# Kernel tuning notes

Hardware: AMD Instinct MI355X
Metric: run time of the kernel (lower is better)

## Reference

```python
import jax, jax.numpy as jnp
import numpy as np

B, S, IN_DIM, CTX = 32, 512, 256, 128
D, H, L = 128, 4, 2
DH = D // H
HID = 512
TOTAL = 11 * D * D + 8 * D  # hypernet flat weight size per sample
EPS = 1e-5


def _layernorm(x, g, b):
    mu = jnp.mean(x, axis=-1, keepdims=True)
    var = jnp.mean(jnp.square(x - mu), axis=-1, keepdims=True)
    return (x - mu) * jax.lax.rsqrt(var + EPS) * g + b


def setup_inputs() -> dict:
    key = jax.random.key(0)
    ks = jax.random.split(key, 24)
    f32 = jnp.float32
    inp = {
        'x': jax.random.normal(ks[0], (B, S, IN_DIM), f32),
        'context_vector': jax.random.normal(ks[1], (B, CTX), f32),
        'in_proj_w': jax.random.normal(ks[2], (D, IN_DIM), f32) * (IN_DIM ** -0.5),
        'in_proj_b': jnp.zeros((D,), f32),
        'pe': jax.random.normal(ks[3], (1, S, D), f32) * 0.02,
        'hfc1_w': jax.random.normal(ks[4], (L, HID, CTX), f32) * (CTX ** -0.5),
        'hfc1_b': jnp.zeros((L, HID), f32),
        'hfc2_w': jax.random.normal(ks[5], (L, TOTAL, HID), f32) * 0.02,
        'hfc2_b': jnp.zeros((L, TOTAL), f32),
        'out_proj_w': jax.random.normal(ks[6], (L, D, D), f32) * (D ** -0.5),
        'out_proj_b': jnp.zeros((L, D), f32),
        'ln1_g': jnp.ones((L, D), f32), 'ln1_b': jnp.zeros((L, D), f32),
        'ln2_g': jnp.ones((L, D), f32), 'ln2_b': jnp.zeros((L, D), f32),
        'alpha1': jnp.full((L,), 0.5, f32), 'alpha2': jnp.full((L,), 0.5, f32),
        'head_w': jax.random.normal(ks[7], (1, D), f32) * (D ** -0.5),
        'head_b': jnp.zeros((1,), f32),
    }
    return inp


def reference(x, context_vector, in_proj_w, in_proj_b, pe, hfc1_w, hfc1_b,
              hfc2_w, hfc2_b, out_proj_w, out_proj_b, ln1_g, ln1_b,
              ln2_g, ln2_b, alpha1, alpha2, head_w, head_b):
    # input projection + learned positional encoding
    h = jnp.einsum('bsi,di->bsd', x, in_proj_w) + in_proj_b
    h = h + pe[:, :h.shape[1], :]

    # flat split offsets for hypernet output
    sizes = [3 * D * D, 3 * D, 4 * D * D, 4 * D, 4 * D * D, D]
    offs = np.concatenate([[0], np.cumsum(sizes)])

    for l in range(L):
        # hypernet: per-sample weights from context
        hid = jax.nn.relu(context_vector @ hfc1_w[l].T + hfc1_b[l])
        flat = hid @ hfc2_w[l].T + hfc2_b[l]  # [B, TOTAL]
        aw = flat[:, offs[0]:offs[1]].reshape(B, 3 * D, D)
        ab = flat[:, offs[1]:offs[2]]                     # [B, 3D]
        f1w = flat[:, offs[2]:offs[3]].reshape(B, 4 * D, D)
        f1b = flat[:, offs[3]:offs[4]]                    # [B, 4D]
        f2w = flat[:, offs[4]:offs[5]].reshape(B, D, 4 * D)
        f2b = flat[:, offs[5]:offs[6]]                    # [B, D]

        # per-sample QKV projection (grouped GEMM over batch)
        qkv = jnp.einsum('bsd,bed->bse', h, aw) + ab[:, None, :]
        q, k, v = jnp.split(qkv, 3, axis=-1)
        q = q.reshape(B, S, H, DH)
        k = k.reshape(B, S, H, DH)
        v = v.reshape(B, S, H, DH)
        scores = jnp.einsum('bqhd,bkhd->bhqk', q, k) / jnp.sqrt(jnp.float32(DH))
        attn = jax.nn.softmax(scores, axis=-1)
        ctx = jnp.einsum('bhqk,bkhd->bqhd', attn, v).reshape(B, S, D)
        attn_out = jnp.einsum('bsd,ed->bse', ctx, out_proj_w[l]) + out_proj_b[l]

        h = _layernorm(h + alpha1[l] * attn_out, ln1_g[l], ln1_b[l])

        # per-sample FFN
        ff = jax.nn.relu(jnp.einsum('bsd,bfd->bsf', h, f1w) + f1b[:, None, :])
        ff = jnp.einsum('bsf,bdf->bsd', ff, f2w) + f2b[:, None, :]

        h = _layernorm(h + alpha2[l] * ff, ln2_g[l], ln2_b[l])

    out = h[:, -1, :] @ head_w.T + head_b  # [B, 1]
    return out
```

## Files before the change

### kernel.cpp

```cpp
#include <hip/hip_runtime.h>
#include <hip/hip_bf16.h>

constexpr int B_    = 32;
constexpr int S_    = 512;
constexpr int INDIM = 256;
constexpr int KCTX  = 128;
constexpr int D_    = 128;
constexpr int H_    = 4;
constexpr int L_    = 2;
constexpr int HID_  = 512;
constexpr int TOTAL_ = 11 * D_ * D_ + 8 * D_;
constexpr int OFF_AB  = 3 * D_ * D_;
constexpr int OFF_F1W = OFF_AB + 3 * D_;
constexpr int OFF_F1B = OFF_F1W + 4 * D_ * D_;
constexpr int OFF_F2W = OFF_F1B + 4 * D_;
constexpr int OFF_F2B = OFF_F2W + 4 * D_ * D_;
constexpr int TP = 132;

typedef __attribute__((ext_vector_type(8))) short short8;
typedef __attribute__((ext_vector_type(4))) short short4v;
typedef __attribute__((ext_vector_type(2))) short short2v;
typedef __attribute__((ext_vector_type(4))) float f32x4;

#define MFMA16 __builtin_amdgcn_mfma_f32_16x16x32_bf16

__device__ __forceinline__ short f2bf(float f) {
  __hip_bfloat16 h = __float2bfloat16(f);
  return __builtin_bit_cast(short, h);
}
__device__ __forceinline__ float bf2f(short s) {
  __hip_bfloat16 h = __builtin_bit_cast(__hip_bfloat16, s);
  return __bfloat162float(h);
}
struct bfpair { short hi, lo; };
__device__ __forceinline__ bfpair split2p(float x) {
  bfpair p;
  p.hi = f2bf(x);
  p.lo = f2bf(x - bf2f(p.hi));
  return p;
}

__device__ __forceinline__ void cvt_body(const float* __restrict__ in,
                                         short* __restrict__ oh,
                                         short* __restrict__ ol,
                                         int ktShift, int n8, int t) {
  if (t >= n8) return;
  int kt = 1 << ktShift;
  int row = t >> ktShift;
  int kc = t & (kt - 1);
  const float* p = in + ((long)row << (ktShift + 3)) + kc * 8;
  float4 v0 = *(const float4*)p;
  float4 v1 = *(const float4*)(p + 4);
  short8 h8, l8; bfpair q;
  q = split2p(v0.x); h8[0] = q.hi; l8[0] = q.lo;
  q = split2p(v0.y); h8[1] = q.hi; l8[1] = q.lo;
  q = split2p(v0.z); h8[2] = q.hi; l8[2] = q.lo;
  q = split2p(v0.w); h8[3] = q.hi; l8[3] = q.lo;
  q = split2p(v1.x); h8[4] = q.hi; l8[4] = q.lo;
  q = split2p(v1.y); h8[5] = q.hi; l8[5] = q.lo;
  q = split2p(v1.z); h8[6] = q.hi; l8[6] = q.lo;
  q = split2p(v1.w); h8[7] = q.hi; l8[7] = q.lo;
  long o = ((long)(row >> 4) * kt + kc) * 128 + (row & 15) * 8;
  *(short8*)(oh + o) = h8;
  *(short8*)(ol + o) = l8;
}

__global__ __launch_bounds__(256) void k_prep(
    const float* __restrict__ x, const float* __restrict__ ipw,
    const float* __restrict__ opw,
    short* __restrict__ xFh, short* __restrict__ xFl,
    short* __restrict__ ipwFh, short* __restrict__ ipwFl,
    short* __restrict__ opwFh, short* __restrict__ opwFl,
    const float* __restrict__ cvec, const float* __restrict__ h1w,
    const float* __restrict__ h1b,
    short* __restrict__ hidFh, short* __restrict__ hidFl) {
  int id = blockIdx.x, tid = threadIdx.x;
  if (id < 2048) {
    cvt_body(x, xFh, xFl, 5, B_ * S_ * INDIM / 8, id * 256 + tid);
  } else if (id < 2064) {
    cvt_body(ipw, ipwFh, ipwFl, 5, D_ * INDIM / 8, (id - 2048) * 256 + tid);
  } else if (id < 2080) {
    cvt_body(opw, opwFh, opwFl, 4, L_ * D_ * D_ / 8, (id - 2064) * 256 + tid);
  } else {
    int hb = id - 2080;
    int l = hb >> 5, b = hb & 31;
    __shared__ float cs[KCTX];
    if (tid < KCTX) cs[tid] = cvec[b * KCTX + tid];
    __syncthreads();
    #pragma unroll
    for (int jj = 0; jj < 2; ++jj) {
      int j = tid + jj * 256;
      const float* wr = h1w + (long)(l * HID_ + j) * KCTX;
      float s = h1b[l * HID_ + j];
      #pragma unroll
      for (int c = 0; c < KCTX; c += 4) {
        float4 cv = *(const float4*)(cs + c);
        float4 wv = *(const float4*)(wr + c);
        s += cv.x * wv.x + cv.y * wv.y + cv.z * wv.z + cv.w * wv.w;
      }
      s = fmaxf(s, 0.f);
      bfpair p = split2p(s);
      long o = (long)l * 32 * HID_ + ((long)(b >> 4) * 64 + (j >> 3)) * 128
             + (b & 15) * 8 + (j & 7);
      hidFh[o] = p.hi;
      hidFl[o] = p.lo;
    }
  }
}

__device__ void inproj_block(int id,
    const short* __restrict__ xFh, const short* __restrict__ xFl,
    const short* __restrict__ ipwFh, const short* __restrict__ ipwFl,
    const float* __restrict__ ipb, const float* __restrict__ pe,
    float* __restrict__ h_f, short* __restrict__ hFh, short* __restrict__ hFl) {
  const int tid = threadIdx.x, wave = tid >> 6, lane = tid & 63;
  const int r = lane & 15, g = lane >> 4;
  const int bx = id >> 5, b = id & 31;
  const int m0 = bx * 64 + (wave & 1) * 32;
  const int n0 = (wave >> 1) * 64;
  const long KT = (long)INDIM * 16;
  const short* pAh = xFh + (long)b * S_ * INDIM + (m0 >> 4) * KT + g * 128 + r * 8;
  const short* pAl = xFl + (long)b * S_ * INDIM + (m0 >> 4) * KT + g * 128 + r * 8;
  const short* pWh = ipwFh + (n0 >> 4) * KT + g * 128 + r * 8;
  const short* pWl = ipwFl + (n0 >> 4) * KT + g * 128 + r * 8;
  f32x4 acc[2][4] = {{{0,0,0,0},{0,0,0,0},{0,0,0,0},{0,0,0,0}},
                     {{0,0,0,0},{0,0,0,0},{0,0,0,0},{0,0,0,0}}};
  for (int kk = 0; kk < INDIM / 32; ++kk) {
    long ko = (long)kk * 512;
    short8 a0h = *(const short8*)(pAh + ko);
    short8 a1h = *(const short8*)(pAh + KT + ko);
    short8 a0l = *(const short8*)(pAl + ko);
    short8 a1l = *(const short8*)(pAl + KT + ko);
    #pragma unroll
    for (int ns = 0; ns < 4; ++ns) {
      short8 wh = *(const short8*)(pWh + ns * KT + ko);
      short8 wl = *(const short8*)(pWl + ns * KT + ko);
      acc[0][ns] = MFMA16(a0h, wl, acc[0][ns], 0, 0, 0);
      acc[0][ns] = MFMA16(a0l, wh, acc[0][ns], 0, 0, 0);
      acc[0][ns] = MFMA16(a0h, wh, acc[0][ns], 0, 0, 0);
      acc[1][ns] = MFMA16(a1h, wl, acc[1][ns], 0, 0, 0);
      acc[1][ns] = MFMA16(a1l, wh, acc[1][ns], 0, 0, 0);
      acc[1][ns] = MFMA16(a1h, wh, acc[1][ns], 0, 0, 0);
    }
  }
  #pragma unroll
  for (int ms = 0; ms < 2; ++ms) {
    #pragma unroll
    for (int ns = 0; ns < 4; ++ns) {
      int ccol = n0 + ns * 16 + r;
      float bv = ipb[ccol];
      #pragma unroll
      for (int reg = 0; reg < 4; ++reg) {
        int crow = m0 + ms * 16 + g * 4 + reg;
        float v = acc[ms][ns][reg] + bv + pe[crow * D_ + ccol];
        h_f[((long)b * S_ + crow) * D_ + ccol] = v;
        long o = (long)b * 65536 + (long)(crow >> 4) * 2048
               + (ccol >> 3) * 128 + (crow & 15) * 8 + (ccol & 7);
        bfpair sp = split2p(v);
        hFh[o] = sp.hi;
        hFl[o] = sp.lo;
      }
    }
  }
}

__global__ __launch_bounds__(256) void k_flat_ip(
    const short* __restrict__ hidh, const short* __restrict__ hidl,
    const float* __restrict__ W, const float* __restrict__ bias,
    short* __restrict__ awh, short* __restrict__ awl,
    short* __restrict__ f1h, short* __restrict__ f1l,
    short* __restrict__ f2h, short* __restrict__ f2l,
    float* __restrict__ ab, float* __restrict__ f1b, float* __restrict__ f2b,
    const short* __restrict__ xFh, const short* __restrict__ xFl,
    const short* __restrict__ ipwFh, const short* __restrict__ ipwFl,
    const float* __restrict__ ipb, const float* __restrict__ pe,
    float* __restrict__ h_f, short* __restrict__ hFh, short* __restrict__ hFl) {
  __shared__ short wls[2][64 * 64];
  const int id = blockIdx.x;
  if (id < 256) {
    inproj_block(id, xFh, xFl, ipwFh, ipwFl, ipb, pe, h_f, hFh, hFl);
    return;
  }
  const int fid = id - 256;
  const int l = fid / 2832;
  const int bxf = fid % 2832;
  hidh += (long)l * 32 * HID_;
  hidl += (long)l * 32 * HID_;
  W    += (long)l * TOTAL_ * HID_;
  bias += (long)l * TOTAL_;
  awh  += (long)l * B_ * 49152;  awl += (long)l * B_ * 49152;
  f1h  += (long)l * B_ * 65536;  f1l += (long)l * B_ * 65536;
  f2h  += (long)l * B_ * 65536;  f2l += (long)l * B_ * 65536;
  ab   += l * B_ * 384;  f1b += l * B_ * 512;  f2b += l * B_ * 128;
  const int tid = threadIdx.x, wave = tid >> 6, lane = tid & 63;
  const int r = lane & 15, g = lane >> 4;
  const int nb0 = bxf * 64;
  const int rr = tid >> 4;
  const int cc = (tid & 15) * 4;
  const float* wbase = W + (long)nb0 * HID_;
  float4 wv[2][4];
  #pragma unroll
  for (int rnd = 0; rnd < 4; ++rnd) {
    wv[0][rnd] = *(const float4*)(wbase + (long)(rnd * 16 + rr) * HID_ + cc);
    wv[1][rnd] = *(const float4*)(wbase + (long)(rnd * 16 + rr) * HID_ + 64 + cc);
  }
  const short* pAh = hidh + g * 128 + r * 8;
  const short* pAl = hidl + g * 128 + r * 8;
  f32x4 acc0 = {0, 0, 0, 0}, acc1 = {0, 0, 0, 0};
  int cur = 0;
  for (int c0 = 0; c0 < 512; c0 += 64) {
    #pragma unroll
    for (int rnd = 0; rnd < 4; ++rnd) {
      int row = rnd * 16 + rr;
      short4v h4, l4; bfpair q;
      q = split2p(wv[cur][rnd].x); h4[0] = q.hi; l4[0] = q.lo;
      q = split2p(wv[cur][rnd].y); h4[1] = q.hi; l4[1] = q.lo;
      q = split2p(wv[cur][rnd].z); h4[2] = q.hi; l4[2] = q.lo;
      q = split2p(wv[cur][rnd].w); h4[3] = q.hi; l4[3] = q.lo;
      int sb = row * 128 + ((cc * 2) ^ ((row & 7) << 4));
      *(short4v*)((char*)&wls[0][0] + sb) = h4;
      *(short4v*)((char*)&wls[1][0] + sb) = l4;
    }
    if (c0 + 128 < 512) {
      #pragma unroll
      for (int rnd = 0; rnd < 4; ++rnd)
        wv[cur][rnd] = *(const float4*)(wbase + (long)(rnd * 16 + rr) * HID_ + (c0 + 128) + cc);
    }
    __syncthreads();
    #pragma unroll
    for (int kk = 0; kk < 2; ++kk) {
      long ao = (long)(c0 * 16) + kk * 512;
      short8 ah0 = *(const short8*)(pAh + ao);
      short8 ah1 = *(const short8*)(pAh + 8192 + ao);
      short8 al0 = *(const short8*)(pAl + ao);
      short8 al1 = *(const short8*)(pAl + 8192 + ao);
      int wrow = wave * 16 + r;
      int wb = wrow * 128 + ((kk * 64 + g * 16) ^ ((r & 7) << 4));
      short8 wh = *(const short8*)((char*)&wls[0][0] + wb);
      short8 wl = *(const short8*)((char*)&wls[1][0] + wb);
      acc0 = MFMA16(ah0, wl, acc0, 0, 0, 0);
      acc0 = MFMA16(al0, wh, acc0, 0, 0, 0);
      acc0 = MFMA16(ah0, wh, acc0, 0, 0, 0);
      acc1 = MFMA16(ah1, wl, acc1, 0, 0, 0);
      acc1 = MFMA16(al1, wh, acc1, 0, 0, 0);
      acc1 = MFMA16(ah1, wh, acc1, 0, 0, 0);
    }
    __syncthreads();
    cur ^= 1;
  }
  constexpr int TPF = 68;
  float* tile = (float*)&wls[0][0];
  {
    float bv = bias[nb0 + wave * 16 + r];
    int col = wave * 16 + r;
    #pragma unroll
    for (int reg = 0; reg < 4; ++reg) {
      tile[(g * 4 + reg) * TPF + col]      = acc0[reg] + bv;
      tile[(g * 4 + reg + 16) * TPF + col] = acc1[reg] + bv;
    }
  }
  __syncthreads();
  {
    int b  = tid >> 3;
    int cg = tid & 7;
    int t0 = nb0 + cg * 8;
    float v[8];
    #pragma unroll
    for (int j = 0; j < 8; ++j) v[j] = tile[b * TPF + cg * 8 + j];
    if (t0 < OFF_AB) {
      int e = t0 >> 7, d = t0 & 127;
      long a = (long)b * 49152 + ((long)(e >> 4) * 16 + (d >> 3)) * 128 + (e & 15) * 8;
      short8 h8, l8; bfpair q;
      #pragma unroll
      for (int j = 0; j < 8; ++j) { q = split2p(v[j]); h8[j] = q.hi; l8[j] = q.lo; }
      *(short8*)(awh + a) = h8;
      *(short8*)(awl + a) = l8;
    } else if (t0 < OFF_F1W) {
      float* dst = ab + b * 384 + (t0 - OFF_AB);
      float4 x0 = {v[0], v[1], v[2], v[3]}, x1 = {v[4], v[5], v[6], v[7]};
      *(float4*)dst = x0; *(float4*)(dst + 4) = x1;
    } else if (t0 < OFF_F1B) {
      int i = t0 - OFF_F1W; int f = i >> 7, d = i & 127;
      long a = (long)b * 65536 + ((long)(f >> 4) * 16 + (d >> 3)) * 128 + (f & 15) * 8;
      short8 h8, l8; bfpair q;
      #pragma unroll
      for (int j = 0; j < 8; ++j) { q = split2p(v[j]); h8[j] = q.hi; l8[j] = q.lo; }
      *(short8*)(f1h + a) = h8;
      *(short8*)(f1l + a) = l8;
    } else if (t0 < OFF_F2W) {
      float* dst = f1b + b * 512 + (t0 - OFF_F1B);
      float4 x0 = {v[0], v[1], v[2], v[3]}, x1 = {v[4], v[5], v[6], v[7]};
      *(float4*)dst = x0; *(float4*)(dst + 4) = x1;
    } else if (t0 < OFF_F2B) {
      int i = t0 - OFF_F2W; int dd = i >> 9, f = i & 511;
      long a = (long)b * 65536 + ((long)(dd >> 4) * 64 + (f >> 3)) * 128 + (dd & 15) * 8;
      short8 h8, l8; bfpair q;
      #pragma unroll
      for (int j = 0; j < 8; ++j) { q = split2p(v[j]); h8[j] = q.hi; l8[j] = q.lo; }
      *(short8*)(f2h + a) = h8;
      *(short8*)(f2l + a) = l8;
    } else {
      float* dst = f2b + b * 128 + (t0 - OFF_F2B);
      float4 x0 = {v[0], v[1], v[2], v[3]}, x1 = {v[4], v[5], v[6], v[7]};
      *(float4*)dst = x0; *(float4*)(dst + 4) = x1;
    }
  }
}

template <int K, int EPI, bool RELU>
__global__ __launch_bounds__(256) void k_gemm(
    const short* __restrict__ Ah, const short* __restrict__ Al, long sA,
    const short* __restrict__ Wh, const short* __restrict__ Wl, long sW,
    const float* __restrict__ biasP, long sB,
    void* __restrict__ p0, void* __restrict__ p1,
    void* __restrict__ p2, void* __restrict__ p3,
    int N,
    const float* __restrict__ lng, const float* __restrict__ lnb,
    const float* __restrict__ lnal, int mOff, int nOff, int mode) {
  extern __shared__ char smem_dyn[];
  const int tid = threadIdx.x, wave = tid >> 6, lane = tid & 63;
  const int r = lane & 15, g = lane >> 4;
  const int b = blockIdx.z;
  int bx, by;
  if (mode == 1) {
    int xx = blockIdx.x;
    if (xx < 16) { bx = xx >> 1; by = 1 + (xx & 1); }
    else         { bx = 7; by = 0; }
  } else {
    bx = blockIdx.x + mOff; by = blockIdx.y + nOff;
  }
  const int m0 = bx * 64 + (wave & 1) * 32;
  const int n0 = by * 128 + (wave >> 1) * 64;
  const long KT = (long)K * 16;
  const short* pAh = Ah + (long)b * sA + (m0 >> 4) * KT + g * 128 + r * 8;
  const short* pAl = Al + (long)b * sA + (m0 >> 4) * KT + g * 128 + r * 8;
  const short* pWh = Wh + (long)b * sW + (n0 >> 4) * KT + g * 128 + r * 8;
  const short* pWl = Wl + (long)b * sW + (n0 >> 4) * KT + g * 128 + r * 8;
  f32x4 acc[2][4] = {{{0,0,0,0},{0,0,0,0},{0,0,0,0},{0,0,0,0}},
                     {{0,0,0,0},{0,0,0,0},{0,0,0,0},{0,0,0,0}}};
  for (int kk = 0; kk < K / 32; ++kk) {
    long ko = (long)kk * 512;
    short8 a0h = *(const short8*)(pAh + ko);
    short8 a1h = *(const short8*)(pAh + KT + ko);
    short8 a0l = *(const short8*)(pAl + ko);
    short8 a1l = *(const short8*)(pAl + KT + ko);
    #pragma unroll
    for (int ns = 0; ns < 4; ++ns) {
      short8 wh = *(const short8*)(pWh + ns * KT + ko);
      short8 wl = *(const short8*)(pWl + ns * KT + ko);
      acc[0][ns] = MFMA16(a0h, wl, acc[0][ns], 0, 0, 0);
      acc[0][ns] = MFMA16(a0l, wh, acc[0][ns], 0, 0, 0);
      acc[0][ns] = MFMA16(a0h, wh, acc[0][ns], 0, 0, 0);
      acc[1][ns] = MFMA16(a1h, wl, acc[1][ns], 0, 0, 0);
      acc[1][ns] = MFMA16(a1l, wh, acc[1][ns], 0, 0, 0);
      acc[1][ns] = MFMA16(a1h, wh, acc[1][ns], 0, 0, 0);
    }
  }

  if constexpr (EPI == 5) {
    if (by == 2) {
      #pragma unroll
      for (int ms = 0; ms < 2; ++ms) {
        int crow0 = m0 + ms * 16 + g * 4;
        #pragma unroll
        for (int ns = 0; ns < 4; ++ns) {
          int ccol = n0 + ns * 16 + r;
          float bv = biasP[(long)b * sB + ccol];
          int c2 = ccol - 256, hd = c2 >> 5, dd = c2 & 31;
          short4v h4, l4; bfpair q;
          #pragma unroll
          for (int reg = 0; reg < 4; ++reg) {
            float v = acc[ms][ns][reg] + bv;
            q = split2p(v); h4[reg] = q.hi; l4[reg] = q.lo;
          }
          long o = (long)(b * 4 + hd) * 16384 + (dd >> 4) * 8192
                 + (crow0 >> 3) * 128 + (dd & 15) * 8 + (crow0 & 7);
          *(short4v*)((short*)p2 + o) = h4;
          *(short4v*)((short*)p3 + o) = l4;
        }
      }
      return;
    }
  }

  float* tile = (float*)smem_dyn;
  #pragma unroll
  for (int ms = 0; ms < 2; ++ms) {
    #pragma unroll
    for (int ns = 0; ns < 4; ++ns) {
      int ccol = n0 + ns * 16 + r;
      float bv = biasP[(long)b * sB + ccol];
      #pragma unroll
      for (int reg = 0; reg < 4; ++reg) {
        float v = acc[ms][ns][reg] + bv;
        if constexpr (RELU) v = fmaxf(v, 0.f);
        int trow2 = (wave & 1) * 32 + ms * 16 + g * 4 + reg;
        int tcol = (wave >> 1) * 64 + ns * 16 + r;
        tile[trow2 * TP + tcol] = v;
      }
    }
  }
  __syncthreads();

  if constexpr (EPI == 0 || EPI == 5) {
    int row = tid >> 2, cg = tid & 3;
    int crow = bx * 64 + row;
    long rowbase = (long)b * 512 * N + (long)(crow >> 4) * (16 * (long)N) + (crow & 15) * 8;
    #pragma unroll
    for (int j4 = 0; j4 < 4; ++j4) {
      int tcol = j4 * 32 + cg * 8;
      float4 aa = *(const float4*)&tile[row * TP + tcol];
      float4 bb = *(const float4*)&tile[row * TP + tcol + 4];
      short8 h8, l8; bfpair q;
      q = split2p(aa.x); h8[0] = q.hi; l8[0] = q.lo;
      q = split2p(aa.y); h8[1] = q.hi; l8[1] = q.lo;
      q = split2p(aa.z); h8[2] = q.hi; l8[2] = q.lo;
      q = split2p(aa.w); h8[3] = q.hi; l8[3] = q.lo;
      q = split2p(bb.x); h8[4] = q.hi; l8[4] = q.lo;
      q = split2p(bb.y); h8[5] = q.hi; l8[5] = q.lo;
      q = split2p(bb.z); h8[6] = q.hi; l8[6] = q.lo;
      q = split2p(bb.w); h8[7] = q.hi; l8[7] = q.lo;
      int ccol = by * 128 + tcol;
      long o = rowbase + (long)(ccol >> 3) * 128;
      *(short8*)((short*)p0 + o) = h8;
      *(short8*)((short*)p1 + o) = l8;
    }
  } else if constexpr (EPI == 4) {
    int row = tid >> 2, q = tid & 3;
    int brow = bx * 64 + row;
    float a = lnal[0];
    float* hf = (float*)p0;
    float* hrow = hf + ((long)b * S_ + brow) * D_ + q * 32;
    float tv[32];
    float s = 0.f, ss = 0.f;
    #pragma unroll
    for (int i = 0; i < 32; i += 4) {
      float4 hv = *(const float4*)(hrow + i);
      float4 yv = *(const float4*)&tile[row * TP + q * 32 + i];
      float t0 = hv.x + a * yv.x, t1 = hv.y + a * yv.y;
      float t2 = hv.z + a * yv.z, t3 = hv.w + a * yv.w;
      tv[i] = t0; tv[i+1] = t1; tv[i+2] = t2; tv[i+3] = t3;
      s += t0 + t1 + t2 + t3;
      ss += t0*t0 + t1*t1 + t2*t2 + t3*t3;
    }
    s  += __shfl_xor(s, 1);  s  += __shfl_xor(s, 2);
    ss += __shfl_xor(ss, 1); ss += __shfl_xor(ss, 2);
    float mu = s * (1.f / 128.f);
    float varv = ss * (1.f / 128.f) - mu * mu;
    float inv = rsqrtf(varv + 1e-5f);
    short* ph = (short*)p1; short* pl = (short*)p2;
    long fb = (long)b * 65536 + (long)(brow >> 4) * 2048 + (brow & 15) * 8;
    #pragma unroll
    for (int j = 0; j < 4; ++j) {
      short8 hv8, lv8;
      #pragma unroll
      for (int e = 0; e < 8; e += 4) {
        int i = j * 8 + e;
        int c = q * 32 + i;
        float4 gv = *(const float4*)(lng + c);
        float4 bb = *(const float4*)(lnb + c);
        float4 o4;
        o4.x = (tv[i]   - mu) * inv * gv.x + bb.x;
        o4.y = (tv[i+1] - mu) * inv * gv.y + bb.y;
        o4.z = (tv[i+2] - mu) * inv * gv.z + bb.z;
        o4.w = (tv[i+3] - mu) * inv * gv.w + bb.w;
        *(float4*)(hrow + i) = o4;
        bfpair q0 = split2p(o4.x); hv8[e]   = q0.hi; lv8[e]   = q0.lo;
        bfpair q1 = split2p(o4.y); hv8[e+1] = q1.hi; lv8[e+1] = q1.lo;
        bfpair q2 = split2p(o4.z); hv8[e+2] = q2.hi; lv8[e+2] = q2.lo;
        bfpair q3 = split2p(o4.w); hv8[e+3] = q3.hi; lv8[e+3] = q3.lo;
      }
      long o = fb + (q * 4 + j) * 128;
      *(short8*)(ph + o) = hv8;
      *(short8*)(pl + o) = lv8;
    }
  }
}

__global__ __launch_bounds__(128) void k_attn(const short* __restrict__ qkh,
                                              const short* __restrict__ qkl,
                                              const short* __restrict__ vth,
                                              const short* __restrict__ vtl,
                                              short* __restrict__ ch,
                                              short* __restrict__ cl,
                                              int mOff) {
  __shared__ __align__(16) float scr[16][516];
  __shared__ __align__(16) float obuf[16][34];
  const int tid = threadIdx.x, wave = tid >> 6, lane = tid & 63;
  const int r = lane & 15, g = lane >> 4;
  const int b = blockIdx.z, hh = blockIdx.y;
  const int m0 = (blockIdx.x + mOff) * 16;
  const long qb = (long)b * 131072;
  const long qoff = qb + (long)(m0 >> 4) * 4096 + (hh * 4 + g) * 128 + r * 8;
  short8 qh = *(const short8*)(qkh + qoff);
  short8 ql = *(const short8*)(qkl + qoff);
  const float sc = 0.17677669529663687f;
  for (int n0 = wave * 256; n0 < wave * 256 + 256; n0 += 16) {
    long koff = qb + (long)(n0 >> 4) * 4096 + (16 + hh * 4 + g) * 128 + r * 8;
    short8 kh = *(const short8*)(qkh + koff);
    short8 kl = *(const short8*)(qkl + koff);
    f32x4 s = {0, 0, 0, 0};
    s = MFMA16(qh, kl, s, 0, 0, 0);
    s = MFMA16(ql, kh, s, 0, 0, 0);
    s = MFMA16(qh, kh, s, 0, 0, 0);
    #pragma unroll
    for (int reg = 0; reg < 4; ++reg)
      scr[g * 4 + reg][n0 + r] = s[reg] * sc;
  }
  __syncthreads();
  for (int row = wave * 8; row < wave * 8 + 8; ++row) {
    float v[8];
    #pragma unroll
    for (int i = 0; i < 8; ++i) v[i] = scr[row][lane + i * 64];
    float m = v[0];
    #pragma unroll
    for (int i = 1; i < 8; ++i) m = fmaxf(m, v[i]);
    #pragma unroll
    for (int o = 32; o > 0; o >>= 1) m = fmaxf(m, __shfl_xor(m, o));
    float ssum = 0.f;
    #pragma unroll
    for (int i = 0; i < 8; ++i) { v[i] = __expf(v[i] - m); ssum += v[i]; }
    #pragma unroll
    for (int o = 32; o > 0; o >>= 1) ssum += __shfl_xor(ssum, o);
    float inv = 1.f / ssum;
    #pragma unroll
    for (int i = 0; i < 8; ++i) scr[row][lane + i * 64] = v[i] * inv;
  }
  __syncthreads();
  f32x4 o0 = {0, 0, 0, 0}, o1 = {0, 0, 0, 0};
  const long vb = (long)(b * 4 + hh) * 16384;
  for (int kt = wave * 8; kt < wave * 8 + 8; ++kt) {
    float4 pv0 = *(const float4*)&scr[r][kt * 32 + g * 8];
    float4 pv1 = *(const float4*)&scr[r][kt * 32 + g * 8 + 4];
    short8 pah, pal;
    bfpair p;
    p = split2p(pv0.x); pah[0] = p.hi; pal[0] = p.lo;
    p = split2p(pv0.y); pah[1] = p.hi; pal[1] = p.lo;
    p = split2p(pv0.z); pah[2] = p.hi; pal[2] = p.lo;
    p = split2p(pv0.w); pah[3] = p.hi; pal[3] = p.lo;
    p = split2p(pv1.x); pah[4] = p.hi; pal[4] = p.lo;
    p = split2p(pv1.y); pah[5] = p.hi; pal[5] = p.lo;
    p = split2p(pv1.z); pah[6] = p.hi; pal[6] = p.lo;
    p = split2p(pv1.w); pah[7] = p.hi; pal[7] = p.lo;
    long vo = vb + (long)(kt * 4 + g) * 128 + r * 8;
    short8 vh0 = *(const short8*)(vth + vo);
    short8 vh1 = *(const short8*)(vth + vo + 8192);
    short8 vl0 = *(const short8*)(vtl + vo);
    short8 vl1 = *(const short8*)(vtl + vo + 8192);
    o0 = MFMA16(pah, vl0, o0, 0, 0, 0);
    o0 = MFMA16(pal, vh0, o0, 0, 0, 0);
    o0 = MFMA16(pah, vh0, o0, 0, 0, 0);
    o1 = MFMA16(pah, vl1, o1, 0, 0, 0);
    o1 = MFMA16(pal, vh1, o1, 0, 0, 0);
    o1 = MFMA16(pah, vh1, o1, 0, 0, 0);
  }
  if (wave == 1) {
    #pragma unroll
    for (int reg = 0; reg < 4; ++reg) {
      obuf[g * 4 + reg][r] = o0[reg];
      obuf[g * 4 + reg][17 + r] = o1[reg];
    }
  }
  __syncthreads();
  if (wave == 0) {
    #pragma unroll
    for (int reg = 0; reg < 4; ++reg) {
      float a0 = o0[reg] + obuf[g * 4 + reg][r];
      float a1 = o1[reg] + obuf[g * 4 + reg][17 + r];
      int srow = m0 + g * 4 + reg;
      int col0 = hh * 32 + r;
      long o = (long)b * 65536 + (long)(srow >> 4) * 2048
             + (col0 >> 3) * 128 + (srow & 15) * 8 + (col0 & 7);
      bfpair sp0 = split2p(a0);
      ch[o] = sp0.hi; cl[o] = sp0.lo;
      long o2 = o + 2 * 128;
      bfpair sp1 = split2p(a1);
      ch[o2] = sp1.hi; cl[o2] = sp1.lo;
    }
  }
}

__global__ __launch_bounds__(64) void k_head(const float* __restrict__ h,
                                             const float* __restrict__ hw,
                                             const float* __restrict__ hb,
                                             float* __restrict__ out) {
  int b = blockIdx.x, lane = threadIdx.x;
  const float* hr = h + ((long)b * S_ + (S_ - 1)) * D_;
  float v = hr[lane] * hw[lane] + hr[lane + 64] * hw[lane + 64];
  #pragma unroll
  for (int o = 32; o > 0; o >>= 1) v += __shfl_xor(v, o);
  if (lane == 0) out[b] = v + hb[0];
}

extern "C" void kernel_launch(void* const* d_in, const int* in_sizes, int n_in,
                              void* d_out, int out_size, void* d_ws, size_t ws_size,
                              hipStream_t stream) {
  const float* x    = (const float*)d_in[0];
  const float* cvec = (const float*)d_in[1];
  const float* ipw  = (const float*)d_in[2];
  const float* ipb  = (const float*)d_in[3];
  const float* pe   = (const float*)d_in[4];
  const float* h1w  = (const float*)d_in[5];
  const float* h1b  = (const float*)d_in[6];
  const float* h2w  = (const float*)d_in[7];
  const float* h2b  = (const float*)d_in[8];
  const float* opw  = (const float*)d_in[9];
  const float* opb  = (const float*)d_in[10];
  const float* ln1g = (const float*)d_in[11];
  const float* ln1b = (const float*)d_in[12];
  const float* ln2g = (const float*)d_in[13];
  const float* ln2b = (const float*)d_in[14];
  const float* a1   = (const float*)d_in[15];
  const float* a2   = (const float*)d_in[16];
  const float* hw   = (const float*)d_in[17];
  const float* hb   = (const float*)d_in[18];
  float* out = (float*)d_out;

  char* ws = (char*)d_ws;
  size_t off = 0;
  auto alloc = [&](size_t n) { void* p = ws + off; off = (off + n + 255) & ~(size_t)255; return p; };

  const long AWs = (long)B_ * 49152;
  const long F1s = (long)B_ * 65536;
  const long F2s = (long)B_ * 65536;

  short* ff1h  = (short*)alloc((size_t)B_ * S_ * 512 * 2);
  short* ff1l  = (short*)alloc((size_t)B_ * S_ * 512 * 2);
  short* xFh   = ff1h;
  short* xFl   = ff1l;
  float* h_f   = (float*)alloc((size_t)B_ * S_ * D_ * 4);
  short* hFh   = (short*)alloc((size_t)B_ * S_ * D_ * 2);
  short* hFl   = (short*)alloc((size_t)B_ * S_ * D_ * 2);
  short* hidFh = (short*)alloc((size_t)L_ * 32 * HID_ * 2);
  short* hidFl = (short*)alloc((size_t)L_ * 32 * HID_ * 2);
  short* awFh  = (short*)alloc((size_t)L_ * AWs * 2);
  short* awFl  = (short*)alloc((size_t)L_ * AWs * 2);
  short* f1wFh = (short*)alloc((size_t)L_ * F1s * 2);
  short* f1wFl = (short*)alloc((size_t)L_ * F1s * 2);
  short* f2wFh = (short*)alloc((size_t)L_ * F2s * 2);
  short* f2wFl = (short*)alloc((size_t)L_ * F2s * 2);
  float* abF   = (float*)alloc((size_t)L_ * B_ * 384 * 4);
  float* f1bF  = (float*)alloc((size_t)L_ * B_ * 512 * 4);
  float* f2bF  = (float*)alloc((size_t)L_ * B_ * 128 * 4);
  short* qkFh  = (short*)alloc((size_t)B_ * S_ * 256 * 2);
  short* qkFl  = (short*)alloc((size_t)B_ * S_ * 256 * 2);
  short* vtFh  = (short*)alloc((size_t)B_ * H_ * 32 * S_ * 2);
  short* vtFl  = (short*)alloc((size_t)B_ * H_ * 32 * S_ * 2);
  short* cxFh  = (short*)alloc((size_t)B_ * S_ * D_ * 2);
  short* cxFl  = (short*)alloc((size_t)B_ * S_ * D_ * 2);
  short* ipwFh = (short*)alloc((size_t)D_ * INDIM * 2);
  short* ipwFl = (short*)alloc((size_t)D_ * INDIM * 2);
  short* opwFh = (short*)alloc((size_t)L_ * D_ * D_ * 2);
  short* opwFl = (short*)alloc((size_t)L_ * D_ * D_ * 2);

  k_prep<<<2144, 256, 0, stream>>>(x, ipw, opw, xFh, xFl, ipwFh, ipwFl,
                                   opwFh, opwFl, cvec, h1w, h1b, hidFh, hidFl);

  k_flat_ip<<<256 + 2 * 2832, 256, 0, stream>>>(
      hidFh, hidFl, h2w, h2b, awFh, awFl, f1wFh, f1wFl, f2wFh, f2wFl,
      abF, f1bF, f2bF,
      xFh, xFl, ipwFh, ipwFl, ipb, pe, h_f, hFh, hFl);

  constexpr size_t TILE_LDS = 64 * TP * 4;

  {
    int l = 0;
    k_gemm<D_, 5, false><<<dim3(8, 3, B_), 256, TILE_LDS, stream>>>(
        hFh, hFl, (long)S_ * D_, awFh + l * AWs, awFl + l * AWs, 49152,
        abF + l * B_ * 384, 384,
        qkFh, qkFl, vtFh, vtFl, 256, nullptr, nullptr, nullptr, 0, 0, 0);
    k_attn<<<dim3(S_ / 16, H_, B_), 128, 0, stream>>>(qkFh, qkFl, vtFh, vtFl, cxFh, cxFl, 0);
    k_gemm<D_, 4, false><<<dim3(8, 1, B_), 256, TILE_LDS, stream>>>(
        cxFh, cxFl, (long)S_ * D_, opwFh + l * 16384, opwFl + l * 16384, 0,
        opb + l * D_, 0, h_f, hFh, hFl, nullptr, 128,
        ln1g + l * D_, ln1b + l * D_, a1 + l, 0, 0, 0);
    k_gemm<D_, 0, true><<<dim3(8, 4, B_), 256, TILE_LDS, stream>>>(
        hFh, hFl, (long)S_ * D_, f1wFh + l * F1s, f1wFl + l * F1s, 65536,
        f1bF + l * B_ * 512, 512,
        ff1h, ff1l, nullptr, nullptr, 512, nullptr, nullptr, nullptr, 0, 0, 0);
    k_gemm<512, 4, false><<<dim3(8, 1, B_), 256, TILE_LDS, stream>>>(
        ff1h, ff1l, (long)S_ * 512, f2wFh + l * F2s, f2wFl + l * F2s, 65536,
        f2bF + l * B_ * 128, 128,
        h_f, hFh, hFl, nullptr, 128,
        ln2g + l * D_, ln2b + l * D_, a2 + l, 0, 0, 0);
  }

  {
    int l = 1;
    k_gemm<D_, 5, false><<<dim3(17, 1, B_), 256, TILE_LDS, stream>>>(
        hFh, hFl, (long)S_ * D_, awFh + l * AWs, awFl + l * AWs, 49152,
        abF + l * B_ * 384, 384,
        qkFh, qkFl, vtFh, vtFl, 256, nullptr, nullptr, nullptr, 0, 0, 1);
    k_attn<<<dim3(1, H_, B_), 128, 0, stream>>>(qkFh, qkFl, vtFh, vtFl, cxFh, cxFl, 31);
    k_gemm<D_, 4, false><<<dim3(1, 1, B_), 256, TILE_LDS, stream>>>(
        cxFh, cxFl, (long)S_ * D_, opwFh + l * 16384, opwFl + l * 16384, 0,
        opb + l * D_, 0, h_f, hFh, hFl, nullptr, 128,
        ln1g + l * D_, ln1b + l * D_, a1 + l, 7, 0, 0);
    k_gemm<D_, 0, true><<<dim3(1, 4, B_), 256, TILE_LDS, stream>>>(
        hFh, hFl, (long)S_ * D_, f1wFh + l * F1s, f1wFl + l * F1s, 65536,
        f1bF + l * B_ * 512, 512,
        ff1h, ff1l, nullptr, nullptr, 512, nullptr, nullptr, nullptr, 7, 0, 0);
    k_gemm<512, 4, false><<<dim3(1, 1, B_), 256, TILE_LDS, stream>>>(
        ff1h, ff1l, (long)S_ * 512, f2wFh + l * F2s, f2wFl + l * F2s, 65536,
        f2bF + l * B_ * 128, 128,
        h_f, hFh, hFl, nullptr, 128,
        ln2g + l * D_, ln2b + l * D_, a2 + l, 7, 0, 0);
  }
  k_head<<<B_, 64, 0, stream>>>(h_f, hw, hb, out);
}
```

Baseline: 440.2 us.

## Fuse x bf16 split conversion into in-projection GEMM via double-buffered LDS

Drops the separate conversion pass that turned x into hi/lo bf16 fragments in k_prep. The in-projection blocks now load fp32 x directly, split it on the fly into swizzled LDS tiles and feed MFMA from there. The LDS buffer is doubled so the hypernet path also ping-pongs between two buffers. This removes a full write and re-read of the 16MB x fragments, at the cost of more LDS per block (32KB) and extra syncs in the in-projection blocks.

```diff
diff --git a/kernel.cpp b/kernel.cpp
--- a/kernel.cpp
+++ b/kernel.cpp
@@ -66,23 +66,19 @@
 }
 
 __global__ __launch_bounds__(256) void k_prep(
-    const float* __restrict__ x, const float* __restrict__ ipw,
-    const float* __restrict__ opw,
-    short* __restrict__ xFh, short* __restrict__ xFl,
+    const float* __restrict__ ipw, const float* __restrict__ opw,
     short* __restrict__ ipwFh, short* __restrict__ ipwFl,
     short* __restrict__ opwFh, short* __restrict__ opwFl,
     const float* __restrict__ cvec, const float* __restrict__ h1w,
     const float* __restrict__ h1b,
     short* __restrict__ hidFh, short* __restrict__ hidFl) {
   int id = blockIdx.x, tid = threadIdx.x;
-  if (id < 2048) {
-    cvt_body(x, xFh, xFl, 5, B_ * S_ * INDIM / 8, id * 256 + tid);
-  } else if (id < 2064) {
-    cvt_body(ipw, ipwFh, ipwFl, 5, D_ * INDIM / 8, (id - 2048) * 256 + tid);
-  } else if (id < 2080) {
-    cvt_body(opw, opwFh, opwFl, 4, L_ * D_ * D_ / 8, (id - 2064) * 256 + tid);
+  if (id < 16) {
+    cvt_body(ipw, ipwFh, ipwFl, 5, D_ * INDIM / 8, id * 256 + tid);
+  } else if (id < 32) {
+    cvt_body(opw, opwFh, opwFl, 4, L_ * D_ * D_ / 8, (id - 16) * 256 + tid);
   } else {
-    int hb = id - 2080;
+    int hb = id - 32;
     int l = hb >> 5, b = hb & 31;
     __shared__ float cs[KCTX];
     if (tid < KCTX) cs[tid] = cvec[b * KCTX + tid];
@@ -108,62 +104,6 @@
   }
 }
 
-__device__ void inproj_block(int id,
-    const short* __restrict__ xFh, const short* __restrict__ xFl,
-    const short* __restrict__ ipwFh, const short* __restrict__ ipwFl,
-    const float* __restrict__ ipb, const float* __restrict__ pe,
-    float* __restrict__ h_f, short* __restrict__ hFh, short* __restrict__ hFl) {
-  const int tid = threadIdx.x, wave = tid >> 6, lane = tid & 63;
-  const int r = lane & 15, g = lane >> 4;
-  const int bx = id >> 5, b = id & 31;
-  const int m0 = bx * 64 + (wave & 1) * 32;
-  const int n0 = (wave >> 1) * 64;
-  const long KT = (long)INDIM * 16;
-  const short* pAh = xFh + (long)b * S_ * INDIM + (m0 >> 4) * KT + g * 128 + r * 8;
-  const short* pAl = xFl + (long)b * S_ * INDIM + (m0 >> 4) * KT + g * 128 + r * 8;
-  const short* pWh = ipwFh + (n0 >> 4) * KT + g * 128 + r * 8;
-  const short* pWl = ipwFl + (n0 >> 4) * KT + g * 128 + r * 8;
-  f32x4 acc[2][4] = {{{0,0,0,0},{0,0,0,0},{0,0,0,0},{0,0,0,0}},
-                     {{0,0,0,0},{0,0,0,0},{0,0,0,0},{0,0,0,0}}};
-  for (int kk = 0; kk < INDIM / 32; ++kk) {
-    long ko = (long)kk * 512;
-    short8 a0h = *(const short8*)(pAh + ko);
-    short8 a1h = *(const short8*)(pAh + KT + ko);
-    short8 a0l = *(const short8*)(pAl + ko);
-    short8 a1l = *(const short8*)(pAl + KT + ko);
-    #pragma unroll
-    for (int ns = 0; ns < 4; ++ns) {
-      short8 wh = *(const short8*)(pWh + ns * KT + ko);
-      short8 wl = *(const short8*)(pWl + ns * KT + ko);
-      acc[0][ns] = MFMA16(a0h, wl, acc[0][ns], 0, 0, 0);
-      acc[0][ns] = MFMA16(a0l, wh, acc[0][ns], 0, 0, 0);
-      acc[0][ns] = MFMA16(a0h, wh, acc[0][ns], 0, 0, 0);
-      acc[1][ns] = MFMA16(a1h, wl, acc[1][ns], 0, 0, 0);
-      acc[1][ns] = MFMA16(a1l, wh, acc[1][ns], 0, 0, 0);
-      acc[1][ns] = MFMA16(a1h, wh, acc[1][ns], 0, 0, 0);
-    }
-  }
-  #pragma unroll
-  for (int ms = 0; ms < 2; ++ms) {
-    #pragma unroll
-    for (int ns = 0; ns < 4; ++ns) {
-      int ccol = n0 + ns * 16 + r;
-      float bv = ipb[ccol];
-      #pragma unroll
-      for (int reg = 0; reg < 4; ++reg) {
-        int crow = m0 + ms * 16 + g * 4 + reg;
-        float v = acc[ms][ns][reg] + bv + pe[crow * D_ + ccol];
-        h_f[((long)b * S_ + crow) * D_ + ccol] = v;
-        long o = (long)b * 65536 + (long)(crow >> 4) * 2048
-               + (ccol >> 3) * 128 + (crow & 15) * 8 + (ccol & 7);
-        bfpair sp = split2p(v);
-        hFh[o] = sp.hi;
-        hFl[o] = sp.lo;
-      }
-    }
-  }
-}
-
 __global__ __launch_bounds__(256) void k_flat_ip(
     const short* __restrict__ hidh, const short* __restrict__ hidl,
     const float* __restrict__ W, const float* __restrict__ bias,
@@ -171,16 +111,98 @@
     short* __restrict__ f1h, short* __restrict__ f1l,
     short* __restrict__ f2h, short* __restrict__ f2l,
     float* __restrict__ ab, float* __restrict__ f1b, float* __restrict__ f2b,
-    const short* __restrict__ xFh, const short* __restrict__ xFl,
+    const float* __restrict__ x,
     const short* __restrict__ ipwFh, const short* __restrict__ ipwFl,
     const float* __restrict__ ipb, const float* __restrict__ pe,
     float* __restrict__ h_f, short* __restrict__ hFh, short* __restrict__ hFl) {
-  __shared__ short wls[2][64 * 64];
+  __shared__ short wls[2][2][64 * 64];
   const int id = blockIdx.x;
+  const int tid = threadIdx.x, wave = tid >> 6, lane = tid & 63;
+  const int r = lane & 15, g = lane >> 4;
+  const int rr = tid >> 4;
+  const int cc = (tid & 15) * 4;
+
   if (id < 256) {
-    inproj_block(id, xFh, xFl, ipwFh, ipwFl, ipb, pe, h_f, hFh, hFl);
+    const int bx = id >> 5, b = id & 31;
+    const float* abase = x + ((long)b * S_ + bx * 64) * INDIM;
+    float4 av[2][4];
+    #pragma unroll
+    for (int rnd = 0; rnd < 4; ++rnd) {
+      av[0][rnd] = *(const float4*)(abase + (long)(rnd * 16 + rr) * INDIM + cc);
+      av[1][rnd] = *(const float4*)(abase + (long)(rnd * 16 + rr) * INDIM + 64 + cc);
+    }
+    const int n0 = (wave >> 1) * 64;
+    const short* pWh = ipwFh + (n0 >> 4) * 4096 + g * 128 + r * 8;
+    const short* pWl = ipwFl + (n0 >> 4) * 4096 + g * 128 + r * 8;
+    f32x4 acc[2][4] = {{{0,0,0,0},{0,0,0,0},{0,0,0,0},{0,0,0,0}},
+                       {{0,0,0,0},{0,0,0,0},{0,0,0,0},{0,0,0,0}}};
+    for (int i = 0; i < 4; ++i) {
+      int c0 = i * 64, cur = i & 1;
+      #pragma unroll
+      for (int rnd = 0; rnd < 4; ++rnd) {
+        int row = rnd * 16 + rr;
+        short4v h4, l4; bfpair q;
+        q = split2p(av[cur][rnd].x); h4[0] = q.hi; l4[0] = q.lo;
+        q = split2p(av[cur][rnd].y); h4[1] = q.hi; l4[1] = q.lo;
+        q = split2p(av[cur][rnd].z); h4[2] = q.hi; l4[2] = q.lo;
+        q = split2p(av[cur][rnd].w); h4[3] = q.hi; l4[3] = q.lo;
+        int sb = row * 128 + ((cc * 2) ^ ((row & 7) << 4));
+        *(short4v*)((char*)&wls[cur][0][0] + sb) = h4;
+        *(short4v*)((char*)&wls[cur][1][0] + sb) = l4;
+      }
+      if (i + 2 < 4) {
+        #pragma unroll
+        for (int rnd = 0; rnd < 4; ++rnd)
+          av[cur][rnd] = *(const float4*)(abase + (long)(rnd * 16 + rr) * INDIM + (c0 + 128) + cc);
+      }
+      __syncthreads();
+      #pragma unroll
+      for (int kk = 0; kk < 2; ++kk) {
+        long wo = (long)(c0 * 16) + kk * 512;
+        short8 ah[2], al[2];
+        #pragma unroll
+        for (int ms = 0; ms < 2; ++ms) {
+          int arow = (wave & 1) * 32 + ms * 16 + r;
+          int abyte = arow * 128 + ((kk * 64 + g * 16) ^ ((r & 7) << 4));
+          ah[ms] = *(const short8*)((char*)&wls[cur][0][0] + abyte);
+          al[ms] = *(const short8*)((char*)&wls[cur][1][0] + abyte);
+        }
+        #pragma unroll
+        for (int ns = 0; ns < 4; ++ns) {
+          short8 wh = *(const short8*)(pWh + ns * 4096 + wo);
+          short8 wl = *(const short8*)(pWl + ns * 4096 + wo);
+          #pragma unroll
+          for (int ms = 0; ms < 2; ++ms) {
+            acc[ms][ns] = MFMA16(ah[ms], wl, acc[ms][ns], 0, 0, 0);
+            acc[ms][ns] = MFMA16(al[ms], wh, acc[ms][ns], 0, 0, 0);
+            acc[ms][ns] = MFMA16(ah[ms], wh, acc[ms][ns], 0, 0, 0);
+          }
+        }
+      }
+      __syncthreads();
+    }
+    #pragma unroll
+    for (int ms = 0; ms < 2; ++ms) {
+      #pragma unroll
+      for (int ns = 0; ns < 4; ++ns) {
+        int ccol = n0 + ns * 16 + r;
+        float bv = ipb[ccol];
+        #pragma unroll
+        for (int reg = 0; reg < 4; ++reg) {
+          int crow = bx * 64 + (wave & 1) * 32 + ms * 16 + g * 4 + reg;
+          float v = acc[ms][ns][reg] + bv + pe[crow * D_ + ccol];
+          h_f[((long)b * S_ + crow) * D_ + ccol] = v;
+          long o = (long)b * 65536 + (long)(crow >> 4) * 2048
+                 + (ccol >> 3) * 128 + (crow & 15) * 8 + (ccol & 7);
+          bfpair sp = split2p(v);
+          hFh[o] = sp.hi;
+          hFl[o] = sp.lo;
+        }
+      }
+    }
     return;
   }
+
   const int fid = id - 256;
   const int l = fid / 2832;
   const int bxf = fid % 2832;
@@ -192,11 +214,7 @@
   f1h  += (long)l * B_ * 65536;  f1l += (long)l * B_ * 65536;
   f2h  += (long)l * B_ * 65536;  f2l += (long)l * B_ * 65536;
   ab   += l * B_ * 384;  f1b += l * B_ * 512;  f2b += l * B_ * 128;
-  const int tid = threadIdx.x, wave = tid >> 6, lane = tid & 63;
-  const int r = lane & 15, g = lane >> 4;
   const int nb0 = bxf * 64;
-  const int rr = tid >> 4;
-  const int cc = (tid & 15) * 4;
   const float* wbase = W + (long)nb0 * HID_;
   float4 wv[2][4];
   #pragma unroll
@@ -207,8 +225,8 @@
   const short* pAh = hidh + g * 128 + r * 8;
   const short* pAl = hidl + g * 128 + r * 8;
   f32x4 acc0 = {0, 0, 0, 0}, acc1 = {0, 0, 0, 0};
-  int cur = 0;
-  for (int c0 = 0; c0 < 512; c0 += 64) {
+  for (int i = 0; i < 8; ++i) {
+    int c0 = i * 64, cur = i & 1;
     #pragma unroll
     for (int rnd = 0; rnd < 4; ++rnd) {
       int row = rnd * 16 + rr;
@@ -218,10 +236,10 @@
       q = split2p(wv[cur][rnd].z); h4[2] = q.hi; l4[2] = q.lo;
       q = split2p(wv[cur][rnd].w); h4[3] = q.hi; l4[3] = q.lo;
       int sb = row * 128 + ((cc * 2) ^ ((row & 7) << 4));
-      *(short4v*)((char*)&wls[0][0] + sb) = h4;
-      *(short4v*)((char*)&wls[1][0] + sb) = l4;
-    }
-    if (c0 + 128 < 512) {
+      *(short4v*)((char*)&wls[cur][0][0] + sb) = h4;
+      *(short4v*)((char*)&wls[cur][1][0] + sb) = l4;
+    }
+    if (i + 2 < 8) {
       #pragma unroll
       for (int rnd = 0; rnd < 4; ++rnd)
         wv[cur][rnd] = *(const float4*)(wbase + (long)(rnd * 16 + rr) * HID_ + (c0 + 128) + cc);
@@ -236,8 +254,8 @@
       short8 al1 = *(const short8*)(pAl + 8192 + ao);
       int wrow = wave * 16 + r;
       int wb = wrow * 128 + ((kk * 64 + g * 16) ^ ((r & 7) << 4));
-      short8 wh = *(const short8*)((char*)&wls[0][0] + wb);
-      short8 wl = *(const short8*)((char*)&wls[1][0] + wb);
+      short8 wh = *(const short8*)((char*)&wls[cur][0][0] + wb);
+      short8 wl = *(const short8*)((char*)&wls[cur][1][0] + wb);
       acc0 = MFMA16(ah0, wl, acc0, 0, 0, 0);
       acc0 = MFMA16(al0, wh, acc0, 0, 0, 0);
       acc0 = MFMA16(ah0, wh, acc0, 0, 0, 0);
@@ -246,10 +264,9 @@
       acc1 = MFMA16(ah1, wh, acc1, 0, 0, 0);
     }
     __syncthreads();
-    cur ^= 1;
   }
   constexpr int TPF = 68;
-  float* tile = (float*)&wls[0][0];
+  float* tile = (float*)&wls[0][0][0];
   {
     float bv = bias[nb0 + wave * 16 + r];
     int col = wave * 16 + r;
@@ -626,8 +643,6 @@
 
   short* ff1h  = (short*)alloc((size_t)B_ * S_ * 512 * 2);
   short* ff1l  = (short*)alloc((size_t)B_ * S_ * 512 * 2);
-  short* xFh   = ff1h;
-  short* xFl   = ff1l;
   float* h_f   = (float*)alloc((size_t)B_ * S_ * D_ * 4);
   short* hFh   = (short*)alloc((size_t)B_ * S_ * D_ * 2);
   short* hFl   = (short*)alloc((size_t)B_ * S_ * D_ * 2);
@@ -653,13 +668,13 @@
   short* opwFh = (short*)alloc((size_t)L_ * D_ * D_ * 2);
   short* opwFl = (short*)alloc((size_t)L_ * D_ * D_ * 2);
 
-  k_prep<<<2144, 256, 0, stream>>>(x, ipw, opw, xFh, xFl, ipwFh, ipwFl,
-                                   opwFh, opwFl, cvec, h1w, h1b, hidFh, hidFl);
+  k_prep<<<96, 256, 0, stream>>>(ipw, opw, ipwFh, ipwFl, opwFh, opwFl,
+                                 cvec, h1w, h1b, hidFh, hidFl);
 
   k_flat_ip<<<256 + 2 * 2832, 256, 0, stream>>>(
       hidFh, hidFl, h2w, h2b, awFh, awFl, f1wFh, f1wFl, f2wFh, f2wFl,
       abF, f1bF, f2bF,
-      xFh, xFl, ipwFh, ipwFl, ipb, pe, h_f, hFh, hFl);
+      x, ipwFh, ipwFl, ipb, pe, h_f, hFh, hFl);
 
   constexpr size_t TILE_LDS = 64 * TP * 4;
 
```

Result: faster. 417.1 us (-5.2%).
